# Kernel tuning notes

Hardware: AMD Instinct MI355X
Metric: run time of the kernel (lower is better)

The kernel has to match this reference:

```python
import jax, jax.numpy as jnp
import numpy as np

N_NODES = 100000
N_EDGES = 3200000
N_FEAT = 128
N_HID = 64


def gcn_conv(x, src, dst, ew, W, b, n):
    # x: [N, Fin]; src/dst: [E'] incl. self-loops; ew: [E'] edge weights
    xw = x @ W  # [N, Fout]
    deg = jax.ops.segment_sum(ew, dst, num_segments=n)  # [N]
    dinv = jnp.where(deg > 0, jax.lax.rsqrt(jnp.maximum(deg, 1e-12)), 0.0)
    norm = dinv[src] * ew * dinv[dst]  # [E']
    out = jax.ops.segment_sum(norm[:, None] * xw[src], dst, num_segments=n)
    return out + b


def setup_inputs() -> dict:
    key = jax.random.key(0)
    k = jax.random.split(key, 8)
    x = jax.random.normal(k[0], (N_NODES, N_FEAT), dtype=jnp.float32)
    edge_index = jax.random.randint(k[1], (2, N_EDGES), 0, N_NODES, dtype=jnp.int32)
    edge_attr = jax.random.uniform(k[2], (N_EDGES,), dtype=jnp.float32)
    s1 = 1.0 / np.sqrt(N_FEAT)
    s2 = 1.0 / np.sqrt(N_HID)
    W1 = jax.random.uniform(k[3], (N_FEAT, N_HID), minval=-s1, maxval=s1, dtype=jnp.float32)
    b1 = jnp.zeros((N_HID,), dtype=jnp.float32)
    W2 = jax.random.uniform(k[4], (N_HID, 1), minval=-s2, maxval=s2, dtype=jnp.float32)
    b2 = jnp.zeros((1,), dtype=jnp.float32)
    return {"x": x, "edge_index": edge_index, "edge_attr": edge_attr,
            "W1": W1, "b1": b1, "W2": W2, "b2": b2}


def reference(x, edge_index, edge_attr, W1, b1, W2, b2):
    n = x.shape[0]
    # add self-loops with weight 1 (PyG gcn_norm, improved=False)
    loop = jnp.arange(n, dtype=edge_index.dtype)
    src = jnp.concatenate([edge_index[0], loop])
    dst = jnp.concatenate([edge_index[1], loop])
    ew = jnp.concatenate([edge_attr, jnp.ones((n,), dtype=edge_attr.dtype)])
    h = gcn_conv(x, src, dst, ew, W1, b1, n)
    h = jax.nn.relu(h)
    # dropout is identity in eval mode
    out = gcn_conv(h, src, dst, ew, W2, b2, n)
    return out
```

## Files before the change

### kernel.cpp

```cpp
#include <hip/hip_runtime.h>
#include <hip/hip_fp16.h>


#define NPB_LOG 6
#define NPB     64
#define PCAP    2432
#define MAXPART 1600
#define NEDG    8192

typedef _Float16 f16x8 __attribute__((ext_vector_type(8)));
typedef float    f32x4 __attribute__((ext_vector_type(4)));

__global__ void k_initcur(int* __restrict__ gcur, int npart) {
    int i = blockIdx.x * blockDim.x + threadIdx.x;
    if (i < npart) gcur[i] = i * PCAP;
}

__global__ __launch_bounds__(256) void k_binA(const int* __restrict__ src,
                                              const int* __restrict__ dst,
                                              const float* __restrict__ ea,
                                              int* __restrict__ gcur,
                                              uint2* __restrict__ part,
                                              int E, int npart) {
    __shared__ int hist[MAXPART];
    __shared__ int base[MAXPART];
    int t = threadIdx.x;
    int c0 = blockIdx.x * NEDG;
    for (int i = t; i < npart; i += 256) hist[i] = 0;
    __syncthreads();
    const int ITER = NEDG / 256;
    int dv[ITER];
#pragma unroll
    for (int j = 0; j < ITER; ++j) {
        int e = c0 + j * 256 + t;
        dv[j] = (e < E) ? dst[e] : -1;
        if (dv[j] >= 0) atomicAdd(&hist[dv[j] >> NPB_LOG], 1);
    }
    __syncthreads();
    for (int i = t; i < npart; i += 256) {
        int h = hist[i];
        if (h > 0) base[i] = atomicAdd(&gcur[i], h);
        hist[i] = 0;
    }
    __syncthreads();
#pragma unroll
    for (int j = 0; j < ITER; ++j) {
        if (dv[j] >= 0) {
            int e = c0 + j * 256 + t;
            int b = dv[j] >> NPB_LOG;
            int p = base[b] + atomicAdd(&hist[b], 1);
            if (p < (b + 1) * PCAP)
                part[p] = make_uint2((uint)src[e] | ((uint)(dv[j] & (NPB - 1)) << 17),
                                     __float_as_uint(ea[e]));
        }
    }
}

__global__ __launch_bounds__(256) void k_binB(const int* __restrict__ gcur,
                                              const uint2* __restrict__ part,
                                              int2* __restrict__ ecsr,
                                              int* __restrict__ rowstart,
                                              int* __restrict__ cntg,
                                              float* __restrict__ dinv, int n) {
    __shared__ int   cnt[NPB];
    __shared__ float wsum[NPB];
    __shared__ int   cur[NPB];
    int b = blockIdx.x, t = threadIdx.x;
    if (t < NPB) { cnt[t] = 0; wsum[t] = 0.0f; }
    __syncthreads();
    int beg = b * PCAP;
    int len = gcur[b] - beg;
    if (len > PCAP) len = PCAP;
    for (int j = t; j < len; j += 256) {
        uint2 ed = part[beg + j];
        int dlow = (ed.x >> 17) & (NPB - 1);
        atomicAdd(&cnt[dlow], 1);
        atomicAdd(&wsum[dlow], __uint_as_float(ed.y));
    }
    __syncthreads();
    if (t < 64) {
        int v = cnt[t];
        int s = v;
        for (int off = 1; off < 64; off <<= 1) {
            int u = __shfl_up(s, off, 64);
            if (t >= off) s += u;
        }
        int excl = s - v;
        cur[t] = excl;
        int node = (b << NPB_LOG) + t;
        if (node < n) {
            rowstart[node] = beg + excl;
            cntg[node]     = v;
            dinv[node]     = rsqrtf(1.0f + wsum[t]);
        }
    }
    __syncthreads();
    for (int j = t; j < len; j += 256) {
        uint2 ed = part[beg + j];
        int dlow = (ed.x >> 17) & (NPB - 1);
        int p = atomicAdd(&cur[dlow], 1);
        ecsr[beg + p] = make_int2((int)(ed.x & 0x1FFFF), (int)ed.y);
    }
}

#define XPAD 136
__global__ __launch_bounds__(256) void k_gemm1m(const float* __restrict__ x,
                                                const float* __restrict__ W1,
                                                const float* __restrict__ dinv,
                                                __half* __restrict__ xw2, int n) {
    __shared__ __align__(16) _Float16 xs[64 * XPAD];
    __shared__ __align__(16) _Float16 wt[64 * XPAD];
    int tid = threadIdx.x;
    int row0 = blockIdx.x * 64;
    for (int i = tid; i < 64 * 32; i += 256) {
        int r = i >> 5, k4 = i & 31;
        float4 f = make_float4(0.f, 0.f, 0.f, 0.f);
        int gr = row0 + r;
        if (gr < n) f = ((const float4*)x)[(size_t)gr * 32 + k4];
        union { _Float16 h[4]; uint2 u; } tmp;
        tmp.h[0] = (_Float16)f.x; tmp.h[1] = (_Float16)f.y;
        tmp.h[2] = (_Float16)f.z; tmp.h[3] = (_Float16)f.w;
        *(uint2*)&xs[r * XPAD + k4 * 4] = tmp.u;
    }
    for (int i = tid; i < 128 * 64; i += 256) {
        int k = i >> 6, nn = i & 63;
        wt[nn * XPAD + k] = (_Float16)W1[i];
    }
    __syncthreads();

    int strip = tid >> 6;
    int lane  = tid & 63;
    int quad  = lane >> 4;
    int m     = lane & 15;
    f32x4 acc[4] = {{0,0,0,0},{0,0,0,0},{0,0,0,0},{0,0,0,0}};
#pragma unroll
    for (int kc = 0; kc < 4; ++kc) {
        f16x8 a = *(const f16x8*)&xs[(strip * 16 + m) * XPAD + kc * 32 + quad * 8];
#pragma unroll
        for (int nt = 0; nt < 4; ++nt) {
            f16x8 b = *(const f16x8*)&wt[(nt * 16 + m) * XPAD + kc * 32 + quad * 8];
            acc[nt] = __builtin_amdgcn_mfma_f32_16x16x32_f16(a, b, acc[nt], 0, 0, 0);
        }
    }
    float dv[4];
#pragma unroll
    for (int reg = 0; reg < 4; ++reg) {
        int gr = row0 + strip * 16 + quad * 4 + reg;
        dv[reg] = (gr < n) ? dinv[gr] : 0.0f;
    }
#pragma unroll
    for (int nt = 0; nt < 4; ++nt) {
#pragma unroll
        for (int reg = 0; reg < 4; ++reg) {
            int gr = row0 + strip * 16 + quad * 4 + reg;
            if (gr < n)
                xw2[(size_t)gr * 64 + nt * 16 + m] = __float2half(dv[reg] * acc[nt][reg]);
        }
    }
}

__global__ __launch_bounds__(256) void k_agg1f(const int* __restrict__ rowstart,
                                               const int* __restrict__ cntg,
                                               const int2* __restrict__ ecsr,
                                               const float* __restrict__ dinv,
                                               const __half* __restrict__ xw2,
                                               const float* __restrict__ b1,
                                               const float* __restrict__ W2,
                                               float* __restrict__ g, int n) {
    int i = blockIdx.x * 4 + (threadIdx.x >> 6);
    int lane = threadIdx.x & 63;
    if (i >= n) return;
    size_t beg = (size_t)rowstart[i];
    int len = cntg[i];
    float acc = __half2float(xw2[(size_t)i * 64 + lane]);
    for (int j0 = 0; j0 < len; j0 += 64) {
        int idx = j0 + lane;
        int c = 0; float w = 0.0f;
        if (idx < len) {
            int2 ed = ecsr[beg + idx];
            c = ed.x;
            w = __int_as_float(ed.y);
        }
        int m = min(64, len - j0);
        int j = 0;
        for (; j + 8 <= m; j += 8) {
            int   c0 = __shfl(c, j,     64);
            int   c1 = __shfl(c, j + 1, 64);
            int   c2 = __shfl(c, j + 2, 64);
            int   c3 = __shfl(c, j + 3, 64);
            int   c4 = __shfl(c, j + 4, 64);
            int   c5 = __shfl(c, j + 5, 64);
            int   c6 = __shfl(c, j + 6, 64);
            int   c7 = __shfl(c, j + 7, 64);
            float w0 = __shfl(w, j,     64);
            float w1 = __shfl(w, j + 1, 64);
            float w2 = __shfl(w, j + 2, 64);
            float w3 = __shfl(w, j + 3, 64);
            float w4 = __shfl(w, j + 4, 64);
            float w5 = __shfl(w, j + 5, 64);
            float w6 = __shfl(w, j + 6, 64);
            float w7 = __shfl(w, j + 7, 64);
            float v0 = __half2float(xw2[(size_t)c0 * 64 + lane]);
            float v1 = __half2float(xw2[(size_t)c1 * 64 + lane]);
            float v2 = __half2float(xw2[(size_t)c2 * 64 + lane]);
            float v3 = __half2float(xw2[(size_t)c3 * 64 + lane]);
            float v4 = __half2float(xw2[(size_t)c4 * 64 + lane]);
            float v5 = __half2float(xw2[(size_t)c5 * 64 + lane]);
            float v6 = __half2float(xw2[(size_t)c6 * 64 + lane]);
            float v7 = __half2float(xw2[(size_t)c7 * 64 + lane]);
            acc += w0 * v0; acc += w1 * v1; acc += w2 * v2; acc += w3 * v3;
            acc += w4 * v4; acc += w5 * v5; acc += w6 * v6; acc += w7 * v7;
        }
        for (; j < m; ++j) {
            int   cj = __shfl(c, j, 64);
            float wj = __shfl(w, j, 64);
            acc += wj * __half2float(xw2[(size_t)cj * 64 + lane]);
        }
    }
    float di = dinv[i];
    float h = fmaxf(di * acc + b1[lane], 0.0f) * W2[lane];
    for (int off = 32; off; off >>= 1) h += __shfl_down(h, off, 64);
    if (lane == 0) g[i] = di * h;
}

__global__ __launch_bounds__(256) void k_agg2(const int* __restrict__ rowstart,
                                              const int* __restrict__ cntg,
                                              const int2* __restrict__ ecsr,
                                              const float* __restrict__ dinv,
                                              const float* __restrict__ g,
                                              const float* __restrict__ b2,
                                              float* __restrict__ out, int n) {
    int i = blockIdx.x * 4 + (threadIdx.x >> 6);
    int lane = threadIdx.x & 63;
    if (i >= n) return;
    size_t beg = (size_t)rowstart[i];
    int len = cntg[i];
    float p = 0.0f;
    for (int j = lane; j < len; j += 64) {
        int2 ed = ecsr[beg + j];
        p += __int_as_float(ed.y) * g[ed.x];
    }
    for (int off = 32; off; off >>= 1) p += __shfl_down(p, off, 64);
    if (lane == 0) out[i] = b2[0] + dinv[i] * (g[i] + p);
}

extern "C" void kernel_launch(void* const* d_in, const int* in_sizes, int n_in,
                              void* d_out, int out_size, void* d_ws, size_t ws_size,
                              hipStream_t stream) {
    const float* x  = (const float*)d_in[0];
    const int*   ei = (const int*)  d_in[1];
    const float* ea = (const float*)d_in[2];
    const float* W1 = (const float*)d_in[3];
    const float* b1 = (const float*)d_in[4];
    const float* W2 = (const float*)d_in[5];
    const float* b2 = (const float*)d_in[6];
    float* out = (float*)d_out;

    int n = in_sizes[0] / 128;
    int E = in_sizes[1] / 2;
    const int* src = ei;
    const int* dst = ei + E;
    int npart = (n + NPB - 1) >> NPB_LOG;

    int*    ws       = (int*)d_ws;
    int*    gcur     = ws;
    uint2*  part     = (uint2*)(ws + MAXPART);
    __half* xw2      = (__half*)part;
    size_t  psz      = (size_t)npart * PCAP;
    int2*   ecsr     = (int2*)(ws + MAXPART + psz * 2);
    int*    rowstart = ws + MAXPART + psz * 4;
    int*    cntg     = rowstart + n;
    float*  dinv     = (float*)(cntg + n);
    float*  g        = dinv + n;

    k_initcur<<<(npart + 255) / 256, 256, 0, stream>>>(gcur, npart);
    k_binA  <<<(E + NEDG - 1) / NEDG, 256, 0, stream>>>(src, dst, ea, gcur, part, E, npart);
    k_binB  <<<npart, 256, 0, stream>>>(gcur, part, ecsr, rowstart, cntg, dinv, n);
    k_gemm1m<<<(n + 63) / 64, 256, 0, stream>>>(x, W1, dinv, xw2, n);
    k_agg1f <<<(n + 3) / 4, 256, 0, stream>>>(rowstart, cntg, ecsr, dinv, xw2, b1, W2, g, n);
    k_agg2  <<<(n + 3) / 4, 256, 0, stream>>>(rowstart, cntg, ecsr, dinv, g, b2, out, n);
}
```

Baseline: 356.0 us.

## Drop global CSR build; sort partitions in shared memory inside aggregation kernels

Removes the global CSR array (ecsr/rowstart/cntg). Degree computation becomes a slim kernel. Layer-1 aggregation now re-sorts each 64-node partition into LDS per block before gathering. Layer-2 aggregation reads the unsorted partition directly and uses shared atomics. This avoids writing and re-reading the CSR array in global memory, and NEDG is halved so binning launches more blocks. The trade-offs are a 19KB LDS staging buffer per block, which lowers occupancy, fewer and larger blocks for layer 1 with imbalance across 16 serial nodes per wave, and shared-atomic contention in layer 2.

```diff
diff --git a/kernel.cpp b/kernel.cpp
--- a/kernel.cpp
+++ b/kernel.cpp
@@ -6,7 +6,7 @@
 #define NPB     64
 #define PCAP    2432
 #define MAXPART 1600
-#define NEDG    8192
+#define NEDG    4096
 
 typedef _Float16 f16x8 __attribute__((ext_vector_type(8)));
 typedef float    f32x4 __attribute__((ext_vector_type(4)));
@@ -56,51 +56,23 @@
     }
 }
 
-__global__ __launch_bounds__(256) void k_binB(const int* __restrict__ gcur,
-                                              const uint2* __restrict__ part,
-                                              int2* __restrict__ ecsr,
-                                              int* __restrict__ rowstart,
-                                              int* __restrict__ cntg,
-                                              float* __restrict__ dinv, int n) {
-    __shared__ int   cnt[NPB];
+__global__ __launch_bounds__(256) void k_deg(const int* __restrict__ gcur,
+                                             const uint2* __restrict__ part,
+                                             float* __restrict__ dinv, int n) {
     __shared__ float wsum[NPB];
-    __shared__ int   cur[NPB];
     int b = blockIdx.x, t = threadIdx.x;
-    if (t < NPB) { cnt[t] = 0; wsum[t] = 0.0f; }
+    if (t < NPB) wsum[t] = 0.0f;
     __syncthreads();
     int beg = b * PCAP;
     int len = gcur[b] - beg;
     if (len > PCAP) len = PCAP;
     for (int j = t; j < len; j += 256) {
         uint2 ed = part[beg + j];
-        int dlow = (ed.x >> 17) & (NPB - 1);
-        atomicAdd(&cnt[dlow], 1);
-        atomicAdd(&wsum[dlow], __uint_as_float(ed.y));
-    }
-    __syncthreads();
-    if (t < 64) {
-        int v = cnt[t];
-        int s = v;
-        for (int off = 1; off < 64; off <<= 1) {
-            int u = __shfl_up(s, off, 64);
-            if (t >= off) s += u;
-        }
-        int excl = s - v;
-        cur[t] = excl;
-        int node = (b << NPB_LOG) + t;
-        if (node < n) {
-            rowstart[node] = beg + excl;
-            cntg[node]     = v;
-            dinv[node]     = rsqrtf(1.0f + wsum[t]);
-        }
-    }
-    __syncthreads();
-    for (int j = t; j < len; j += 256) {
-        uint2 ed = part[beg + j];
-        int dlow = (ed.x >> 17) & (NPB - 1);
-        int p = atomicAdd(&cur[dlow], 1);
-        ecsr[beg + p] = make_int2((int)(ed.x & 0x1FFFF), (int)ed.y);
-    }
+        atomicAdd(&wsum[(ed.x >> 17) & (NPB - 1)], __uint_as_float(ed.y));
+    }
+    __syncthreads();
+    int node = (b << NPB_LOG) + t;
+    if (t < NPB && node < n) dinv[node] = rsqrtf(1.0f + wsum[t]);
 }
 
 #define XPAD 136
@@ -159,89 +131,128 @@
     }
 }
 
-__global__ __launch_bounds__(256) void k_agg1f(const int* __restrict__ rowstart,
-                                               const int* __restrict__ cntg,
-                                               const int2* __restrict__ ecsr,
+__global__ __launch_bounds__(256) void k_aggS1(const int* __restrict__ gcur,
+                                               const uint2* __restrict__ part,
                                                const float* __restrict__ dinv,
                                                const __half* __restrict__ xw2,
                                                const float* __restrict__ b1,
                                                const float* __restrict__ W2,
                                                float* __restrict__ g, int n) {
-    int i = blockIdx.x * 4 + (threadIdx.x >> 6);
-    int lane = threadIdx.x & 63;
-    if (i >= n) return;
-    size_t beg = (size_t)rowstart[i];
-    int len = cntg[i];
-    float acc = __half2float(xw2[(size_t)i * 64 + lane]);
-    for (int j0 = 0; j0 < len; j0 += 64) {
-        int idx = j0 + lane;
-        int c = 0; float w = 0.0f;
-        if (idx < len) {
-            int2 ed = ecsr[beg + idx];
-            c = ed.x;
-            w = __int_as_float(ed.y);
-        }
-        int m = min(64, len - j0);
-        int j = 0;
-        for (; j + 8 <= m; j += 8) {
-            int   c0 = __shfl(c, j,     64);
-            int   c1 = __shfl(c, j + 1, 64);
-            int   c2 = __shfl(c, j + 2, 64);
-            int   c3 = __shfl(c, j + 3, 64);
-            int   c4 = __shfl(c, j + 4, 64);
-            int   c5 = __shfl(c, j + 5, 64);
-            int   c6 = __shfl(c, j + 6, 64);
-            int   c7 = __shfl(c, j + 7, 64);
-            float w0 = __shfl(w, j,     64);
-            float w1 = __shfl(w, j + 1, 64);
-            float w2 = __shfl(w, j + 2, 64);
-            float w3 = __shfl(w, j + 3, 64);
-            float w4 = __shfl(w, j + 4, 64);
-            float w5 = __shfl(w, j + 5, 64);
-            float w6 = __shfl(w, j + 6, 64);
-            float w7 = __shfl(w, j + 7, 64);
-            float v0 = __half2float(xw2[(size_t)c0 * 64 + lane]);
-            float v1 = __half2float(xw2[(size_t)c1 * 64 + lane]);
-            float v2 = __half2float(xw2[(size_t)c2 * 64 + lane]);
-            float v3 = __half2float(xw2[(size_t)c3 * 64 + lane]);
-            float v4 = __half2float(xw2[(size_t)c4 * 64 + lane]);
-            float v5 = __half2float(xw2[(size_t)c5 * 64 + lane]);
-            float v6 = __half2float(xw2[(size_t)c6 * 64 + lane]);
-            float v7 = __half2float(xw2[(size_t)c7 * 64 + lane]);
-            acc += w0 * v0; acc += w1 * v1; acc += w2 * v2; acc += w3 * v3;
-            acc += w4 * v4; acc += w5 * v5; acc += w6 * v6; acc += w7 * v7;
-        }
-        for (; j < m; ++j) {
-            int   cj = __shfl(c, j, 64);
-            float wj = __shfl(w, j, 64);
-            acc += wj * __half2float(xw2[(size_t)cj * 64 + lane]);
-        }
-    }
-    float di = dinv[i];
-    float h = fmaxf(di * acc + b1[lane], 0.0f) * W2[lane];
-    for (int off = 32; off; off >>= 1) h += __shfl_down(h, off, 64);
-    if (lane == 0) g[i] = di * h;
-}
-
-__global__ __launch_bounds__(256) void k_agg2(const int* __restrict__ rowstart,
-                                              const int* __restrict__ cntg,
-                                              const int2* __restrict__ ecsr,
+    __shared__ uint2 stag[PCAP];
+    __shared__ int cnt[NPB], sbeg[NPB], cur[NPB];
+    int b = blockIdx.x, t = threadIdx.x;
+    int lane = t & 63, wv = t >> 6;
+    if (t < NPB) cnt[t] = 0;
+    __syncthreads();
+    int beg = b * PCAP;
+    int len = gcur[b] - beg;
+    if (len > PCAP) len = PCAP;
+    for (int j = t; j < len; j += 256)
+        atomicAdd(&cnt[(part[beg + j].x >> 17) & (NPB - 1)], 1);
+    __syncthreads();
+    if (t < 64) {
+        int v = cnt[t], s = v;
+        for (int off = 1; off < 64; off <<= 1) {
+            int u = __shfl_up(s, off, 64);
+            if (t >= off) s += u;
+        }
+        sbeg[t] = s - v;
+        cur[t]  = s - v;
+    }
+    __syncthreads();
+    for (int j = t; j < len; j += 256) {
+        uint2 ed = part[beg + j];
+        int p = atomicAdd(&cur[(ed.x >> 17) & (NPB - 1)], 1);
+        stag[p] = make_uint2(ed.x & 0x1FFFF, ed.y);
+    }
+    __syncthreads();
+    float b1v = b1[lane], w2v = W2[lane];
+    int nbase = b << NPB_LOG;
+#pragma unroll 1
+    for (int k = 0; k < 16; ++k) {
+        int r = k * 4 + wv;
+        int node = nbase + r;
+        if (node >= n) continue;
+        int s0 = sbeg[r], lr = cnt[r];
+        float acc = __half2float(xw2[(size_t)node * 64 + lane]);
+        for (int j0 = 0; j0 < lr; j0 += 64) {
+            int idx = j0 + lane;
+            int c = 0; float w = 0.0f;
+            if (idx < lr) {
+                uint2 ed = stag[s0 + idx];
+                c = (int)ed.x;
+                w = __uint_as_float(ed.y);
+            }
+            int m = min(64, lr - j0);
+            int j = 0;
+            for (; j + 8 <= m; j += 8) {
+                int   c0 = __shfl(c, j,     64);
+                int   c1 = __shfl(c, j + 1, 64);
+                int   c2 = __shfl(c, j + 2, 64);
+                int   c3 = __shfl(c, j + 3, 64);
+                int   c4 = __shfl(c, j + 4, 64);
+                int   c5 = __shfl(c, j + 5, 64);
+                int   c6 = __shfl(c, j + 6, 64);
+                int   c7 = __shfl(c, j + 7, 64);
+                float w0 = __shfl(w, j,     64);
+                float w1 = __shfl(w, j + 1, 64);
+                float w2 = __shfl(w, j + 2, 64);
+                float w3 = __shfl(w, j + 3, 64);
+                float w4 = __shfl(w, j + 4, 64);
+                float w5 = __shfl(w, j + 5, 64);
+                float w6 = __shfl(w, j + 6, 64);
+                float w7 = __shfl(w, j + 7, 64);
+                float v0 = __half2float(xw2[(size_t)c0 * 64 + lane]);
+                float v1 = __half2float(xw2[(size_t)c1 * 64 + lane]);
+                float v2 = __half2float(xw2[(size_t)c2 * 64 + lane]);
+                float v3 = __half2float(xw2[(size_t)c3 * 64 + lane]);
+                float v4 = __half2float(xw2[(size_t)c4 * 64 + lane]);
+                float v5 = __half2float(xw2[(size_t)c5 * 64 + lane]);
+                float v6 = __half2float(xw2[(size_t)c6 * 64 + lane]);
+                float v7 = __half2float(xw2[(size_t)c7 * 64 + lane]);
+                acc += w0 * v0; acc += w1 * v1; acc += w2 * v2; acc += w3 * v3;
+                acc += w4 * v4; acc += w5 * v5; acc += w6 * v6; acc += w7 * v7;
+            }
+            for (; j < m; ++j) {
+                int   cj = __shfl(c, j, 64);
+                float wj = __shfl(w, j, 64);
+                acc += wj * __half2float(xw2[(size_t)cj * 64 + lane]);
+            }
+        }
+        float di = dinv[node];
+        float h = fmaxf(di * acc + b1v, 0.0f) * w2v;
+        for (int off = 32; off; off >>= 1) h += __shfl_down(h, off, 64);
+        if (lane == 0) g[node] = di * h;
+    }
+}
+
+__global__ __launch_bounds__(256) void k_agg2(const int* __restrict__ gcur,
+                                              const uint2* __restrict__ part,
                                               const float* __restrict__ dinv,
                                               const float* __restrict__ g,
                                               const float* __restrict__ b2,
                                               float* __restrict__ out, int n) {
-    int i = blockIdx.x * 4 + (threadIdx.x >> 6);
-    int lane = threadIdx.x & 63;
-    if (i >= n) return;
-    size_t beg = (size_t)rowstart[i];
-    int len = cntg[i];
-    float p = 0.0f;
-    for (int j = lane; j < len; j += 64) {
-        int2 ed = ecsr[beg + j];
-        p += __int_as_float(ed.y) * g[ed.x];
-    }
-    for (int off = 32; off; off >>= 1) p += __shfl_down(p, off, 64);
-    if (lane == 0) out[i] = b2[0] + dinv[i] * (g[i] + p);
+    __shared__ float accs[4][NPB];
+    int b = blockIdx.x, t = threadIdx.x;
+    int wv = t >> 6;
+    accs[t >> 6][t & 63] = 0.0f;
+    __syncthreads();
+    int beg = b * PCAP;
+    int len = gcur[b] - beg;
+    if (len > PCAP) len = PCAP;
+    for (int j = t; j < len; j += 256) {
+        uint2 ed = part[beg + j];
+        atomicAdd(&accs[wv][(ed.x >> 17) & (NPB - 1)],
+                  __uint_as_float(ed.y) * g[ed.x & 0x1FFFF]);
+    }
+    __syncthreads();
+    if (t < NPB) {
+        int node = (b << NPB_LOG) + t;
+        if (node < n) {
+            float p = accs[0][t] + accs[1][t] + accs[2][t] + accs[3][t];
+            out[node] = b2[0] + dinv[node] * (g[node] + p);
+        }
+    }
 }
 
 extern "C" void kernel_launch(void* const* d_in, const int* in_sizes, int n_in,
@@ -262,21 +273,18 @@
     const int* dst = ei + E;
     int npart = (n + NPB - 1) >> NPB_LOG;
 
-    int*    ws       = (int*)d_ws;
-    int*    gcur     = ws;
-    uint2*  part     = (uint2*)(ws + MAXPART);
-    __half* xw2      = (__half*)part;
-    size_t  psz      = (size_t)npart * PCAP;
-    int2*   ecsr     = (int2*)(ws + MAXPART + psz * 2);
-    int*    rowstart = ws + MAXPART + psz * 4;
-    int*    cntg     = rowstart + n;
-    float*  dinv     = (float*)(cntg + n);
-    float*  g        = dinv + n;
+    int*    ws   = (int*)d_ws;
+    int*    gcur = ws;
+    uint2*  part = (uint2*)(ws + MAXPART);
+    size_t  psz  = (size_t)npart * PCAP;
+    __half* xw2  = (__half*)(ws + MAXPART + psz * 2);
+    float*  dinv = (float*)(ws + MAXPART + psz * 2 + (size_t)n * 32);
+    float*  g    = dinv + n;
 
     k_initcur<<<(npart + 255) / 256, 256, 0, stream>>>(gcur, npart);
     k_binA  <<<(E + NEDG - 1) / NEDG, 256, 0, stream>>>(src, dst, ea, gcur, part, E, npart);
-    k_binB  <<<npart, 256, 0, stream>>>(gcur, part, ecsr, rowstart, cntg, dinv, n);
+    k_deg   <<<npart, 256, 0, stream>>>(gcur, part, dinv, n);
     k_gemm1m<<<(n + 63) / 64, 256, 0, stream>>>(x, W1, dinv, xw2, n);
-    k_agg1f <<<(n + 3) / 4, 256, 0, stream>>>(rowstart, cntg, ecsr, dinv, xw2, b1, W2, g, n);
-    k_agg2  <<<(n + 3) / 4, 256, 0, stream>>>(rowstart, cntg, ecsr, dinv, g, b2, out, n);
-}
+    k_aggS1 <<<npart, 256, 0, stream>>>(gcur, part, dinv, xw2, b1, W2, g, n);
+    k_agg2  <<<npart, 256, 0, stream>>>(gcur, part, dinv, g, b2, out, n);
+}
```

New measurement: 371.9 us. 4.5% more time.
